# Kernel tuning notes

Measured on AMD Instinct MI355X. Metric: run time of the kernel, lower is better.

Reference implementation:

```python
import jax, jax.numpy as jnp
import numpy as np

VOCAB, DIM, LAYERS, SEQ, BATCH = 32000, 512, 4, 2048, 2
LN_EPS = 1e-5


def _sinusoidal(seq_len, dim):
    pos = jnp.arange(seq_len, dtype=jnp.float32)[:, None]
    div = jnp.exp(jnp.arange(0, dim, 2, dtype=jnp.float32) * (-np.log(10000.0) / dim))
    pe = jnp.zeros((seq_len, dim), jnp.float32)
    pe = pe.at[:, 0::2].set(jnp.sin(pos * div))
    pe = pe.at[:, 1::2].set(jnp.cos(pos * div))
    return pe


def _layernorm(x, w, b):
    mu = jnp.mean(x, axis=-1, keepdims=True)
    var = jnp.mean(jnp.square(x - mu), axis=-1, keepdims=True)
    return (x - mu) * jax.lax.rsqrt(var + LN_EPS) * w + b


def _tpi(h, Wo, bo, iscale, Wm, bm, Wout, bout):
    # h: [B,S,D]
    omega = jnp.einsum('bsd,de->bse', h, Wo) + bo
    magnitude = jax.nn.sigmoid(jnp.einsum('bsd,de->bse', h, Wm) + bm) * 5.0
    phi = jnp.cumsum(omega * jnp.abs(iscale), axis=1)
    cos_phi = jnp.cos(phi)
    sin_phi = jnp.sin(phi)
    weighted = magnitude * h
    mem_r = jnp.cumsum(weighted * cos_phi, axis=1)
    mem_i = jnp.cumsum(weighted * sin_phi, axis=1)
    acc = jnp.cumsum(magnitude, axis=1) + 1e-8
    mem_r = mem_r / acc
    mem_i = mem_i / acc
    retr_r = mem_r * cos_phi + mem_i * sin_phi
    retr_i = mem_i * cos_phi - mem_r * sin_phi
    ctx = jnp.concatenate([h * cos_phi, h * sin_phi, retr_r, retr_i], axis=-1)  # [B,S,4D]
    return h + jnp.einsum('bsf,fd->bsd', ctx, Wout) + bout


def setup_inputs() -> dict:
    key = jax.random.key(0)
    ks = jax.random.split(key, 8)
    xavier = lambda k, sh: jax.random.normal(k, sh, jnp.float32) * np.sqrt(2.0 / (sh[-2] + sh[-1]))
    return {
        'tokens': jax.random.randint(ks[0], (BATCH, SEQ), 0, VOCAB),
        'emb': jax.random.normal(ks[1], (VOCAB, DIM), jnp.float32) * 0.02,
        'ln_w': jnp.ones((LAYERS, DIM), jnp.float32),
        'ln_b': jnp.zeros((LAYERS, DIM), jnp.float32),
        'W_omega': xavier(ks[2], (LAYERS, DIM, DIM)),
        'b_omega': jnp.zeros((LAYERS, DIM), jnp.float32),
        'int_scale': jnp.full((LAYERS, DIM), 0.001, jnp.float32),
        'W_mag': xavier(ks[3], (LAYERS, DIM, DIM)),
        'b_mag': jnp.zeros((LAYERS, DIM), jnp.float32),
        'W_out': xavier(ks[4], (LAYERS, 4 * DIM, DIM)),
        'b_out': jnp.zeros((LAYERS, DIM), jnp.float32),
        'fln_w': jnp.ones((DIM,), jnp.float32),
        'fln_b': jnp.zeros((DIM,), jnp.float32),
        'W_head': xavier(ks[5], (DIM, VOCAB)),
        'b_head': jnp.zeros((VOCAB,), jnp.float32),
    }


def reference(tokens, emb, ln_w, ln_b, W_omega, b_omega, int_scale, W_mag, b_mag,
              W_out, b_out, fln_w, fln_b, W_head, b_head):
    B, S = tokens.shape
    D = emb.shape[1]
    x = emb[tokens] + _sinusoidal(S, D)[None]
    for l in range(W_omega.shape[0]):
        h = _layernorm(x, ln_w[l], ln_b[l])
        x = x + _tpi(h, W_omega[l], b_omega[l], int_scale[l], W_mag[l], b_mag[l], W_out[l], b_out[l])
    x = _layernorm(x, fln_w, fln_b)
    logits = jnp.einsum('bsd,dv->bsv', x, W_head) + b_head
    return logits
```

## Files before the change

### kernel.cpp

```cpp
#include <hip/hip_runtime.h>
#include <hip/hip_bf16.h>
#include <math.h>

constexpr int Bc = 2, Sc = 2048, Dc = 512, Lc = 4, Vc = 32000;
constexpr int Mc = Bc * Sc;
constexpr int NSEG = 64;
constexpr int SEG = Sc / NSEG;
constexpr float LN_EPS = 1e-5f;

typedef __attribute__((ext_vector_type(8))) short short8;
typedef __attribute__((ext_vector_type(4))) float f32x4;

__device__ __forceinline__ void gload_lds16(const __hip_bfloat16* g, __hip_bfloat16* l) {
    __builtin_amdgcn_global_load_lds((const __attribute__((address_space(1))) void*)g,
                                     (__attribute__((address_space(3))) void*)l, 16, 0, 0);
}

__global__ __launch_bounds__(256) void prep_all(const int* __restrict__ tokens,
                                                const float* __restrict__ emb,
                                                const float* __restrict__ ln_w0,
                                                const float* __restrict__ ln_b0,
                                                float* __restrict__ x,
                                                __hip_bfloat16* __restrict__ h16,
                                                const float* __restrict__ Wo,
                                                const float* __restrict__ Wm,
                                                const float* __restrict__ Wout,
                                                const float* __restrict__ Whead,
                                                const float* __restrict__ bo,
                                                const float* __restrict__ bm,
                                                __hip_bfloat16* __restrict__ Tommag,
                                                __hip_bfloat16* __restrict__ Tout,
                                                __hip_bfloat16* __restrict__ Thead,
                                                float* __restrict__ biasp) {
    int bid = blockIdx.x;
    int tx = threadIdx.x, ty = threadIdx.y;
    int t = ty * 32 + tx;
    if (bid < 4096) {
        __shared__ float red[8];
        int row = bid;
        int s = row % Sc;
        int tok = tokens[row];
        const float kc = -9.210340371976184f / (float)Dc;
        float div = expf((float)(2 * t) * kc);
        float ang = (float)s * div;
        const float* e = emb + (size_t)tok * Dc;
        float v0 = e[2 * t]     + sinf(ang);
        float v1 = e[2 * t + 1] + cosf(ang);
        float2 xv; xv.x = v0; xv.y = v1;
        ((float2*)x)[(size_t)row * (Dc / 2) + t] = xv;
        float sum = v0 + v1;
        for (int o = 32; o; o >>= 1) sum += __shfl_down(sum, o);
        if ((t & 63) == 0) red[t >> 6] = sum;
        __syncthreads();
        float mu = (red[0] + red[1] + red[2] + red[3]) * (1.f / (float)Dc);
        float d0 = v0 - mu, d1 = v1 - mu;
        float vs = d0 * d0 + d1 * d1;
        for (int o = 32; o; o >>= 1) vs += __shfl_down(vs, o);
        if ((t & 63) == 0) red[4 + (t >> 6)] = vs;
        __syncthreads();
        float var = (red[4] + red[5] + red[6] + red[7]) * (1.f / (float)Dc);
        float rstd = 1.f / sqrtf(var + LN_EPS);
        __hip_bfloat162 hb;
        hb.x = __float2bfloat16(d0 * rstd * ln_w0[2 * t] + ln_b0[2 * t]);
        hb.y = __float2bfloat16(d1 * rstd * ln_w0[2 * t + 1] + ln_b0[2 * t + 1]);
        ((__hip_bfloat162*)h16)[(size_t)row * (Dc / 2) + t] = hb;
        return;
    }
    bid -= 4096;
    if (bid >= 22144) {
        int l = bid - 22144;
        #pragma unroll
        for (int q = 0; q < 4; ++q) {
            int i = q * 256 + t;
            biasp[l * 1024 + i] = (i < 512) ? bo[l * 512 + i] : bm[l * 512 + i - 512];
        }
        return;
    }
    const float* ip;
    __hip_bfloat16* op;
    int C, LD, r0, c0;
    if (bid < 1024) {
        int l = bid >> 8, rem = bid & 255;
        ip = Wo + (size_t)l * Dc * Dc;
        op = Tommag + (size_t)l * 1024 * Dc;
        C = Dc; LD = Dc;
        r0 = (rem >> 4) * 32; c0 = (rem & 15) * 32;
    } else if (bid < 2048) {
        int b2 = bid - 1024;
        int l = b2 >> 8, rem = b2 & 255;
        ip = Wm + (size_t)l * Dc * Dc;
        op = Tommag + (size_t)l * 1024 * Dc + (size_t)512 * Dc;
        C = Dc; LD = Dc;
        r0 = (rem >> 4) * 32; c0 = (rem & 15) * 32;
    } else if (bid < 6144) {
        int b2 = bid - 2048;
        int l = b2 >> 10, rem = b2 & 1023;
        ip = Wout + (size_t)l * 4 * Dc * Dc;
        op = Tout + (size_t)l * Dc * 4 * Dc;
        C = Dc; LD = 4 * Dc;
        r0 = (rem >> 4) * 32; c0 = (rem & 15) * 32;
    } else {
        int b2 = bid - 6144;
        ip = Whead;
        op = Thead;
        C = Vc; LD = Dc;
        r0 = (b2 / 1000) * 32; c0 = (b2 % 1000) * 32;
    }
    __shared__ float tile[32][33];
    #pragma unroll
    for (int q = 0; q < 4; ++q) {
        int r = r0 + ty + q * 8;
        tile[ty + q * 8][tx] = ip[(size_t)r * C + c0 + tx];
    }
    __syncthreads();
    #pragma unroll
    for (int q = 0; q < 4; ++q) {
        int c = c0 + ty + q * 8;
        op[(size_t)c * LD + r0 + tx] = __float2bfloat16(tile[tx][ty + q * 8]);
    }
}

__global__ __launch_bounds__(256) void reduce_ln(const float* __restrict__ part,
                                                 const float* __restrict__ bout,
                                                 float* __restrict__ x,
                                                 const __hip_bfloat16* __restrict__ hres,
                                                 const float* __restrict__ w,
                                                 const float* __restrict__ bb,
                                                 __hip_bfloat16* __restrict__ hout,
                                                 int writeX) {
    __shared__ float red[8];
    int row = blockIdx.x;
    int t = threadIdx.x;
    const size_t MN = (size_t)Mc * Dc;
    size_t o2 = (size_t)row * (Dc / 2) + t;
    float2 p0 = ((const float2*)part)[o2];
    float2 p1 = ((const float2*)part)[MN / 2 + o2];
    float2 p2 = ((const float2*)part)[MN + o2];
    float2 p3 = ((const float2*)part)[3 * (MN / 2) + o2];
    float2 xv = ((const float2*)x)[o2];
    __hip_bfloat162 hb = ((const __hip_bfloat162*)hres)[o2];
    float b0 = bout[2 * t], b1 = bout[2 * t + 1];
    float v0 = xv.x + p0.x + p1.x + p2.x + p3.x + b0 + __bfloat162float(hb.x);
    float v1 = xv.y + p0.y + p1.y + p2.y + p3.y + b1 + __bfloat162float(hb.y);
    if (writeX) {
        float2 nv; nv.x = v0; nv.y = v1;
        ((float2*)x)[o2] = nv;
    }
    float sum = v0 + v1;
    for (int o = 32; o; o >>= 1) sum += __shfl_down(sum, o);
    if ((t & 63) == 0) red[t >> 6] = sum;
    __syncthreads();
    float mu = (red[0] + red[1] + red[2] + red[3]) * (1.f / (float)Dc);
    float d0 = v0 - mu, d1 = v1 - mu;
    float vs = d0 * d0 + d1 * d1;
    for (int o = 32; o; o >>= 1) vs += __shfl_down(vs, o);
    if ((t & 63) == 0) red[4 + (t >> 6)] = vs;
    __syncthreads();
    float var = (red[4] + red[5] + red[6] + red[7]) * (1.f / (float)Dc);
    float rstd = 1.f / sqrtf(var + LN_EPS);
    __hip_bfloat162 ho;
    ho.x = __float2bfloat16(d0 * rstd * w[2 * t] + bb[2 * t]);
    ho.y = __float2bfloat16(d1 * rstd * w[2 * t + 1] + bb[2 * t + 1]);
    ((__hip_bfloat162*)hout)[o2] = ho;
}

template<int BM, int EPI, int SPLITK = 1>
__global__ __launch_bounds__(256) void gemm_bt(const __hip_bfloat16* __restrict__ A,
                                               const __hip_bfloat16* __restrict__ Bt,
                                               const float* __restrict__ bias,
                                               float* __restrict__ Cf,
                                               __hip_bfloat16* __restrict__ Cb,
                                               int M, int N, int K) {
    __shared__ __hip_bfloat16 As[BM * 64];
    __shared__ __hip_bfloat16 Bs[128 * 64];
    const int tid = threadIdx.x;
    const int lane = tid & 63;
    const int wave = tid >> 6;
    const int wr = wave >> 1, wc = wave & 1;
    int nwg = gridDim.x * gridDim.y;
    int flat = blockIdx.y * gridDim.x + blockIdx.x;
    int cpx = nwg >> 3;
    int swz = (flat & 7) * cpx + (flat >> 3);
    const int m0 = (swz / gridDim.x) * BM;
    const int n0 = (swz % gridDim.x) * 128;
    const int zz = (SPLITK > 1) ? blockIdx.z : 0;
    const int kbeg = zz * (K / SPLITK);
    const int kend = kbeg + K / SPLITK;
    const int fr = lane & 15, fq = lane >> 4;
    constexpr int MI = BM / 32;
    f32x4 acc[MI][4] = {};
    for (int k0 = kbeg; k0 < kend; k0 += 64) {
        #pragma unroll
        for (int q = 0; q < BM / 32; ++q) {
            int c = q * 256 + tid;
            int row = c >> 3, cb = c & 7;
            int gcb = cb ^ (row & 7);
            gload_lds16(A + (size_t)(m0 + row) * K + (k0 + gcb * 8), &As[c * 8]);
        }
        #pragma unroll
        for (int q = 0; q < 4; ++q) {
            int c = q * 256 + tid;
            int row = c >> 3, cb = c & 7;
            int gcb = cb ^ (row & 7);
            gload_lds16(Bt + (size_t)(n0 + row) * K + (k0 + gcb * 8), &Bs[c * 8]);
        }
        __syncthreads();
        #pragma unroll
        for (int ks = 0; ks < 2; ++ks) {
            short8 a[MI], b[4];
            #pragma unroll
            for (int i = 0; i < MI; ++i) {
                int row = wr * (BM / 2) + i * 16 + fr;
                int sb = (ks * 4 + fq) ^ (row & 7);
                a[i] = *(const short8*)&As[row * 64 + sb * 8];
            }
            #pragma unroll
            for (int j = 0; j < 4; ++j) {
                int row = wc * 64 + j * 16 + fr;
                int sb = (ks * 4 + fq) ^ (row & 7);
                b[j] = *(const short8*)&Bs[row * 64 + sb * 8];
            }
            #pragma unroll
            for (int i = 0; i < MI; ++i)
                #pragma unroll
                for (int j = 0; j < 4; ++j)
                    acc[i][j] = __builtin_amdgcn_mfma_f32_16x16x32_bf16(a[i], b[j], acc[i][j], 0, 0, 0);
        }
        __syncthreads();
    }
    float* Cfz = Cf + (size_t)zz * M * N;
    #pragma unroll
    for (int i = 0; i < MI; ++i) {
        int rowb = m0 + wr * (BM / 2) + i * 16 + fq * 4;
        #pragma unroll
        for (int j = 0; j < 4; ++j) {
            int col = n0 + wc * 64 + j * 16 + fr;
            float bv = (EPI == 3) ? 0.f : bias[col];
            #pragma unroll
            for (int t = 0; t < 4; ++t) {
                size_t idx = (size_t)(rowb + t) * N + col;
                float v = acc[i][j][t] + bv;
                if constexpr (EPI == 0) Cf[idx] = v;
                else if constexpr (EPI == 2) Cb[idx] = __float2bfloat16(v);
                else Cfz[idx] = v;
            }
        }
    }
}

__global__ __launch_bounds__(256) void scan_pass1(const __hip_bfloat16* __restrict__ ommag,
                                                  const __hip_bfloat16* __restrict__ h16,
                                                  const float* __restrict__ iscale,
                                                  float* __restrict__ segTot) {
    int td = threadIdx.x;
    int ts = threadIdx.y;
    int d = blockIdx.x * 64 + td;
    int seg = blockIdx.y * 4 + ts;
    int b = blockIdx.z;
    size_t rbase = (size_t)b * Sc + seg * SEG;
    const __hip_bfloat16* om = ommag + rbase * 1024 + d;
    const __hip_bfloat16* mg = om + 512;
    const __hip_bfloat16* hp = h16 + rbase * Dc + d;
    float isc = fabsf(iscale[d]);
    float phi = 0.f, swc = 0.f, sws = 0.f, sacc = 0.f;
    for (int k = 0; k < SEG; ++k) {
        float o = __bfloat162float(om[(size_t)k * 1024]);
        float mp = __bfloat162float(mg[(size_t)k * 1024]);
        float hh = __bfloat162float(hp[(size_t)k * Dc]);
        phi += o * isc;
        float mag = 5.f / (1.f + expf(-mp));
        float sn, cs; sincosf(phi, &sn, &cs);
        float w = mag * hh;
        swc += w * cs; sws += w * sn; sacc += mag;
    }
    float cP, sP; sincosf(phi, &sP, &cP);
    size_t o = (((size_t)b * NSEG + seg) * 6) * Dc + d;
    segTot[o] = phi; segTot[o + Dc] = cP; segTot[o + 2 * Dc] = sP;
    segTot[o + 3 * Dc] = swc; segTot[o + 4 * Dc] = sws; segTot[o + 5 * Dc] = sacc;
}

__global__ __launch_bounds__(256) void scan_pass3(const __hip_bfloat16* __restrict__ ommag,
                                                  const __hip_bfloat16* __restrict__ h16,
                                                  const float* __restrict__ iscale,
                                                  const float* __restrict__ segTot,
                                                  __hip_bfloat16* __restrict__ ctx) {
    __shared__ float Q[4][6][64];
    int td = threadIdx.x;
    int ts = threadIdx.y;
    int d = blockIdx.x * 64 + td;
    int jj = blockIdx.y;
    int seg = jj * 4 + ts;
    int b = blockIdx.z;
    size_t rbase = (size_t)b * Sc + seg * SEG;
    const __hip_bfloat16* om = ommag + rbase * 1024 + d;
    const __hip_bfloat16* mg = om + 512;
    const __hip_bfloat16* hp = h16 + rbase * Dc + d;
    float isc = fabsf(iscale[d]);
    {
        float Pq = 0.f, zr = 1.f, zi = 0.f, Wr = 0.f, Wi = 0.f, Aq = 0.f;
        for (int c = ts * jj; c < (ts + 1) * jj; ++c) {
            size_t o = (((size_t)b * NSEG + c) * 6) * Dc + d;
            float P = segTot[o], cp = segTot[o + Dc], sp = segTot[o + 2 * Dc];
            float wcv = segTot[o + 3 * Dc], wsv = segTot[o + 4 * Dc], acv = segTot[o + 5 * Dc];
            Wr += zr * wcv - zi * wsv;
            Wi += zi * wcv + zr * wsv;
            Aq += acv; Pq += P;
            float nzr = zr * cp - zi * sp;
            float nzi = zi * cp + zr * sp;
            zr = nzr; zi = nzi;
        }
        Q[ts][0][td] = Pq; Q[ts][1][td] = zr; Q[ts][2][td] = zi;
        Q[ts][3][td] = Wr; Q[ts][4][td] = Wi; Q[ts][5][td] = Aq;
    }
    __syncthreads();
    float PHI = 0.f, UR = 0.f, UI = 0.f, AC = 0.f, gzr = 1.f, gzi = 0.f;
    #pragma unroll
    for (int q = 0; q < 4; ++q) {
        float wr = Q[q][3][td], wi = Q[q][4][td];
        UR += gzr * wr - gzi * wi;
        UI += gzi * wr + gzr * wi;
        AC += Q[q][5][td]; PHI += Q[q][0][td];
        float nzr = gzr * Q[q][1][td] - gzi * Q[q][2][td];
        float nzi = gzi * Q[q][1][td] + gzr * Q[q][2][td];
        gzr = nzr; gzi = nzi;
    }
    for (int c = 4 * jj; c < 4 * jj + ts; ++c) {
        size_t o = (((size_t)b * NSEG + c) * 6) * Dc + d;
        float P = segTot[o], cp = segTot[o + Dc], sp = segTot[o + 2 * Dc];
        float wcv = segTot[o + 3 * Dc], wsv = segTot[o + 4 * Dc], acv = segTot[o + 5 * Dc];
        UR += gzr * wcv - gzi * wsv;
        UI += gzi * wcv + gzr * wsv;
        AC += acv; PHI += P;
        float nzr = gzr * cp - gzi * sp;
        float nzi = gzi * cp + gzr * sp;
        gzr = nzr; gzi = nzi;
    }
    float phi = PHI;
    __hip_bfloat16* ctxp = ctx + rbase * (4 * Dc) + d;
    for (int k = 0; k < SEG; ++k) {
        float o = __bfloat162float(om[(size_t)k * 1024]);
        float mp = __bfloat162float(mg[(size_t)k * 1024]);
        float hh = __bfloat162float(hp[(size_t)k * Dc]);
        phi += o * isc;
        float mag = 5.f / (1.f + expf(-mp));
        float sn, cs; sincosf(phi, &sn, &cs);
        float w = mag * hh;
        UR += w * cs; UI += w * sn; AC += mag;
        float inv = 1.f / (AC + 1e-8f);
        float mr = UR * inv, mi = UI * inv;
        float rr = mr * cs + mi * sn;
        float ri = mi * cs - mr * sn;
        size_t oo = (size_t)k * (4 * Dc);
        ctxp[oo]          = __float2bfloat16(hh * cs);
        ctxp[oo + Dc]     = __float2bfloat16(hh * sn);
        ctxp[oo + 2 * Dc] = __float2bfloat16(rr);
        ctxp[oo + 3 * Dc] = __float2bfloat16(ri);
    }
}

extern "C" void kernel_launch(void* const* d_in, const int* in_sizes, int n_in,
                              void* d_out, int out_size, void* d_ws, size_t ws_size,
                              hipStream_t stream) {
    const int*   tokens    = (const int*)d_in[0];
    const float* emb       = (const float*)d_in[1];
    const float* ln_w      = (const float*)d_in[2];
    const float* ln_b      = (const float*)d_in[3];
    const float* W_omega   = (const float*)d_in[4];
    const float* b_omega   = (const float*)d_in[5];
    const float* int_scale = (const float*)d_in[6];
    const float* W_mag     = (const float*)d_in[7];
    const float* b_mag     = (const float*)d_in[8];
    const float* W_out     = (const float*)d_in[9];
    const float* b_out     = (const float*)d_in[10];
    const float* fln_w     = (const float*)d_in[11];
    const float* fln_b     = (const float*)d_in[12];
    const float* W_head    = (const float*)d_in[13];
    const float* b_head    = (const float*)d_in[14];
    float* out = (float*)d_out;

    char* ws = (char*)d_ws;
    size_t off = 0;
    auto alloc = [&](size_t bytes) -> char* {
        char* p = ws + off;
        off += (bytes + 255) / 256 * 256;
        return p;
    };
    const size_t MD = (size_t)Mc * Dc;
    float* x        = (float*)alloc(MD * 4);
    float* part     = (float*)alloc(MD * 4 * 4);
    __hip_bfloat16* ommag16 = (__hip_bfloat16*)alloc(MD * 2 * 2);
    __hip_bfloat16* h16    = (__hip_bfloat16*)alloc(MD * 2);
    __hip_bfloat16* ctx16  = (__hip_bfloat16*)alloc(MD * 4 * 2);
    __hip_bfloat16* xln16  = (__hip_bfloat16*)alloc(MD * 2);
    float* segTot   = (float*)alloc((size_t)Bc * NSEG * 6 * Dc * 4);
    __hip_bfloat16* Wt_ommag = (__hip_bfloat16*)alloc((size_t)Lc * 1024 * Dc * 2);
    __hip_bfloat16* Wt_out   = (__hip_bfloat16*)alloc((size_t)Lc * Dc * 4 * Dc * 2);
    __hip_bfloat16* Wt_head  = (__hip_bfloat16*)alloc((size_t)Vc * Dc * 2);
    float* bias_ommag        = (float*)alloc((size_t)Lc * 1024 * 4);

    prep_all<<<26244, dim3(32, 8), 0, stream>>>(
        tokens, emb, ln_w, ln_b, x, h16,
        W_omega, W_mag, W_out, W_head, b_omega, b_mag,
        Wt_ommag, Wt_out, Wt_head, bias_ommag);

    dim3 scanGrid(Dc / 64, NSEG / 4, Bc);
    dim3 scanBlk(64, 4);
    for (int l = 0; l < Lc; ++l) {
        gemm_bt<128, 2><<<dim3(1024 / 128, Mc / 128), 256, 0, stream>>>(
            h16, Wt_ommag + (size_t)l * 1024 * Dc, bias_ommag + l * 1024, nullptr, ommag16, Mc, 1024, Dc);
        scan_pass1<<<scanGrid, scanBlk, 0, stream>>>(ommag16, h16, int_scale + l * Dc, segTot);
        scan_pass3<<<scanGrid, scanBlk, 0, stream>>>(ommag16, h16, int_scale + l * Dc, segTot, ctx16);
        gemm_bt<128, 3, 4><<<dim3(Dc / 128, Mc / 128, 4), 256, 0, stream>>>(
            ctx16, Wt_out + (size_t)l * Dc * 4 * Dc, nullptr, part, nullptr, Mc, Dc, 4 * Dc);
        const float* wsel = (l + 1 < Lc) ? (ln_w + (l + 1) * Dc) : fln_w;
        const float* bsel = (l + 1 < Lc) ? (ln_b + (l + 1) * Dc) : fln_b;
        __hip_bfloat16* hsel = (l + 1 < Lc) ? h16 : xln16;
        reduce_ln<<<Mc, 256, 0, stream>>>(part, b_out + l * Dc, x, h16, wsel, bsel, hsel,
                                          (l + 1 < Lc) ? 1 : 0);
    }
    gemm_bt<128, 0><<<dim3(Vc / 128, Mc / 128), 256, 0, stream>>>(
        xln16, Wt_head, b_head, out, nullptr, Mc, Vc, Dc);
}
```

Measured before the change: 589.8 us.

## Add 128x256-tile head GEMM with XCD swizzle and fast trig intrinsics in scans

Replaces the vocabulary-projection GEMM with a dedicated kernel that uses 128x256 tiles, XOR-swizzled LDS staging via direct global-to-LDS loads, and a workgroup remap that groups tiles by XCD for better L2 reuse. Each wave computes a 128x64 slice, which raises MFMA work per LDS load. Separately, the scan kernels switch expf/sincosf to the fast __expf/__sincosf intrinsics to cut transcendental cost. The risks are lower precision in the phase trig and higher register pressure from 128 accumulators per thread, with no pipelining of the k-loop.

Measured after the change: 597.6 us. About the same (+1.3%).

```diff
diff --git a/kernel.cpp b/kernel.cpp
--- a/kernel.cpp
+++ b/kernel.cpp
@@ -248,6 +248,77 @@
     }
 }
 
+__global__ __launch_bounds__(256) void gemm_head256(const __hip_bfloat16* __restrict__ A,
+                                                    const __hip_bfloat16* __restrict__ Bt,
+                                                    const float* __restrict__ bias,
+                                                    float* __restrict__ C,
+                                                    int M, int N, int K) {
+    __shared__ __hip_bfloat16 As[128 * 64];
+    __shared__ __hip_bfloat16 Bs[256 * 64];
+    const int tid = threadIdx.x;
+    const int lane = tid & 63;
+    const int wave = tid >> 6;
+    int nwg = gridDim.x * gridDim.y;
+    int flat = blockIdx.y * gridDim.x + blockIdx.x;
+    int cpx = nwg >> 3;
+    int swz = (flat & 7) * cpx + (flat >> 3);
+    const int m0 = (swz / gridDim.x) * 128;
+    const int n0 = (swz % gridDim.x) * 256;
+    const int fr = lane & 15, fq = lane >> 4;
+    f32x4 acc[8][4] = {};
+    for (int k0 = 0; k0 < K; k0 += 64) {
+        #pragma unroll
+        for (int q = 0; q < 4; ++q) {
+            int c = q * 256 + tid;
+            int row = c >> 3, cb = c & 7;
+            int gcb = cb ^ (row & 7);
+            gload_lds16(A + (size_t)(m0 + row) * K + (k0 + gcb * 8), &As[c * 8]);
+        }
+        #pragma unroll
+        for (int q = 0; q < 8; ++q) {
+            int c = q * 256 + tid;
+            int row = c >> 3, cb = c & 7;
+            int gcb = cb ^ (row & 7);
+            gload_lds16(Bt + (size_t)(n0 + row) * K + (k0 + gcb * 8), &Bs[c * 8]);
+        }
+        __syncthreads();
+        #pragma unroll
+        for (int ks = 0; ks < 2; ++ks) {
+            short8 a[8], b[4];
+            #pragma unroll
+            for (int i = 0; i < 8; ++i) {
+                int row = i * 16 + fr;
+                int sb = (ks * 4 + fq) ^ (row & 7);
+                a[i] = *(const short8*)&As[row * 64 + sb * 8];
+            }
+            #pragma unroll
+            for (int j = 0; j < 4; ++j) {
+                int row = wave * 64 + j * 16 + fr;
+                int sb = (ks * 4 + fq) ^ (row & 7);
+                b[j] = *(const short8*)&Bs[row * 64 + sb * 8];
+            }
+            #pragma unroll
+            for (int i = 0; i < 8; ++i)
+                #pragma unroll
+                for (int j = 0; j < 4; ++j)
+                    acc[i][j] = __builtin_amdgcn_mfma_f32_16x16x32_bf16(a[i], b[j], acc[i][j], 0, 0, 0);
+        }
+        __syncthreads();
+    }
+    #pragma unroll
+    for (int i = 0; i < 8; ++i) {
+        int rowb = m0 + i * 16 + fq * 4;
+        #pragma unroll
+        for (int j = 0; j < 4; ++j) {
+            int col = n0 + wave * 64 + j * 16 + fr;
+            float bv = bias[col];
+            #pragma unroll
+            for (int t = 0; t < 4; ++t)
+                C[(size_t)(rowb + t) * N + col] = acc[i][j][t] + bv;
+        }
+    }
+}
+
 __global__ __launch_bounds__(256) void scan_pass1(const __hip_bfloat16* __restrict__ ommag,
                                                   const __hip_bfloat16* __restrict__ h16,
                                                   const float* __restrict__ iscale,
@@ -268,12 +339,12 @@
         float mp = __bfloat162float(mg[(size_t)k * 1024]);
         float hh = __bfloat162float(hp[(size_t)k * Dc]);
         phi += o * isc;
-        float mag = 5.f / (1.f + expf(-mp));
-        float sn, cs; sincosf(phi, &sn, &cs);
+        float mag = 5.f / (1.f + __expf(-mp));
+        float sn, cs; __sincosf(phi, &sn, &cs);
         float w = mag * hh;
         swc += w * cs; sws += w * sn; sacc += mag;
     }
-    float cP, sP; sincosf(phi, &sP, &cP);
+    float cP, sP; __sincosf(phi, &sP, &cP);
     size_t o = (((size_t)b * NSEG + seg) * 6) * Dc + d;
     segTot[o] = phi; segTot[o + Dc] = cP; segTot[o + 2 * Dc] = sP;
     segTot[o + 3 * Dc] = swc; segTot[o + 4 * Dc] = sws; segTot[o + 5 * Dc] = sacc;
@@ -342,8 +413,8 @@
         float mp = __bfloat162float(mg[(size_t)k * 1024]);
         float hh = __bfloat162float(hp[(size_t)k * Dc]);
         phi += o * isc;
-        float mag = 5.f / (1.f + expf(-mp));
-        float sn, cs; sincosf(phi, &sn, &cs);
+        float mag = 5.f / (1.f + __expf(-mp));
+        float sn, cs; __sincosf(phi, &sn, &cs);
         float w = mag * hh;
         UR += w * cs; UI += w * sn; AC += mag;
         float inv = 1.f / (AC + 1e-8f);
@@ -418,6 +489,6 @@
         reduce_ln<<<Mc, 256, 0, stream>>>(part, b_out + l * Dc, x, h16, wsel, bsel, hsel,
                                           (l + 1 < Lc) ? 1 : 0);
     }
-    gemm_bt<128, 0><<<dim3(Vc / 128, Mc / 128), 256, 0, stream>>>(
-        xln16, Wt_head, b_head, out, nullptr, Mc, Vc, Dc);
-}
+    gemm_head256<<<dim3(Vc / 256, Mc / 128), 256, 0, stream>>>(
+        xln16, Wt_head, b_head, out, Mc, Vc, Dc);
+}
```
